# Performance work log

Hardware: AMD Instinct MI355X
Metric: run time of the kernel (lower is better)

Reference implementation:

```python
import jax, jax.numpy as jnp
import numpy as np

# Production-scale dims: CSA layer on a 64x64, 512-channel decoder feature map
B, C, H, W = 8, 512, 64, 64
HOLE = 32  # centered square hole side -> M = 1024 masked points, N = 3072 context points
EPS = 1e-8


def _mask_and_indices():
    m = np.zeros((H, W), np.float32)
    r0, c0 = (H - HOLE) // 2, (W - HOLE) // 2
    m[r0:r0 + HOLE, c0:c0 + HOLE] = 1.0
    flat = m.reshape(-1)
    mask_idx = np.nonzero(flat > 0.5)[0].astype(np.int32)      # masked (hole) flat positions, raster order
    nonmask_idx = np.nonzero(flat <= 0.5)[0].astype(np.int32)  # known (context) flat positions
    return m, nonmask_idx, mask_idx


def setup_inputs() -> dict:
    key = jax.random.key(0)
    x = jax.random.normal(key, (B, C, H, W), dtype=jnp.float32)
    m, nm, mi = _mask_and_indices()
    return {
        "input": x,
        "mask": jnp.asarray(m),
        "nonmask_point_idx": jnp.asarray(nm),
        "mask_point_idx": jnp.asarray(mi),
    }


def _csa(x, nonmask_point_idx, mask_point_idx):
    """Coherent Semantic Attention with 1x1 patches (shift_sz=1, stride=1).

    For each masked location (raster order): find the most-similar context
    patch by cosine similarity, then coherently blend it with the previously
    generated patch, weighted by their respective similarities.
    """
    b, c, h, w = x.shape
    feats = x.reshape(b, c, h * w)                      # [B,C,HW] 1x1 patches
    ctx = feats[:, :, nonmask_point_idx]                # [B,C,N] known/context patches
    msk = feats[:, :, mask_point_idx]                   # [B,C,M] masked patches
    ctx_n = ctx / (jnp.linalg.norm(ctx, axis=1, keepdims=True) + EPS)
    msk_n = msk / (jnp.linalg.norm(msk, axis=1, keepdims=True) + EPS)

    # cross cosine similarity: dominant compute (B*M*N*C)
    cos = jnp.einsum('bcm,bcn->bmn', msk_n, ctx_n)      # [B,M,N]
    maxc = cos.max(axis=-1)                             # [B,M] best context similarity
    amax = cos.argmax(axis=-1)                          # [B,M]
    # gather the best-matching (unnormalized) context patch per masked point
    best = jnp.take_along_axis(ctx.transpose(0, 2, 1), amax[..., None], axis=1)  # [B,M,C]

    xs = (msk_n.transpose(2, 0, 1),   # [M,B,C] normalized masked patches
          best.transpose(1, 0, 2),    # [M,B,C] best context patches
          maxc.T)                     # [M,B]

    def step(prev, inp):
        mn, bst, mx = inp
        prev_n = prev / (jnp.linalg.norm(prev, axis=-1, keepdims=True) + EPS)
        d_ad = jnp.maximum(jnp.sum(mn * prev_n, axis=-1), 0.0)   # [B] coherence with previous generated patch
        cur = (d_ad[:, None] * prev + mx[:, None] * bst) / (d_ad + mx + EPS)[:, None]
        return cur, cur

    # prev initialized to zeros -> d_ad = 0 for the first masked patch (pure context copy)
    _, gen = jax.lax.scan(step, jnp.zeros((b, c), x.dtype), xs)   # [M,B,C]

    out = feats.at[:, :, mask_point_idx].set(gen.transpose(1, 2, 0))
    return out.reshape(b, c, h, w)


def reference(input, mask, nonmask_point_idx, mask_point_idx):
    return _csa(input, nonmask_point_idx, mask_point_idx)
```

## Files before the change

### kernel.cpp

```cpp
#include <hip/hip_runtime.h>
#include <hip/hip_bf16.h>

#define B_   8
#define C_   512
#define HW_  4096
#define M_   1024
#define N_   3072
#define EPS_ 1e-8f

typedef __attribute__((ext_vector_type(4))) float f32x4;
typedef __attribute__((ext_vector_type(8))) short short8;

__global__ void k_norms(const float* __restrict__ x, float* __restrict__ inv_all) {
    int blk = blockIdx.x;
    int b = blk >> 5;
    int chunk = blk & 31;
    int hw = chunk * 128 + threadIdx.x;
    const float* xb = x + (size_t)b * C_ * HW_;
    float acc = 0.f;
#pragma unroll 8
    for (int c = 0; c < C_; ++c) {
        float v = xb[(size_t)c * HW_ + hw];
        acc = fmaf(v, v, acc);
    }
    inv_all[b * HW_ + hw] = 1.0f / (sqrtf(acc) + EPS_);
}

__global__ __launch_bounds__(256) void k_pack(const float* __restrict__ x,
    const int* __restrict__ nm_idx, const int* __restrict__ m_idx,
    const float* __restrict__ inv_all,
    unsigned int* __restrict__ Apk, unsigned int* __restrict__ Bpk,
    float* __restrict__ invM, float* __restrict__ invC)
{
    __shared__ float T[32][513];
    __shared__ int ps[32];
    int blk = blockIdx.x;
    int t = threadIdx.x;
    int isA = blk < 256;
    int b, grp;
    const int* idxarr;
    if (isA) { b = blk >> 5; grp = blk & 31; idxarr = m_idx; }
    else     { int r = blk - 256; b = r / 96; grp = r % 96; idxarr = nm_idx; }
    const float* xb = x + (size_t)b * C_ * HW_;
    if (t < 32) {
        int p = idxarr[grp * 32 + t];
        ps[t] = p;
        float iv = inv_all[b * HW_ + p];
        if (isA) invM[b * 1024 + grp * 32 + t] = iv;
        else     invC[b * 3072 + grp * 32 + t] = iv;
    }
    __syncthreads();
#pragma unroll 4
    for (int rep = 0; rep < 64; ++rep) {
        int idx = rep * 256 + t;
        int c = idx >> 5, i = idx & 31;
        T[i][c] = xb[(size_t)c * HW_ + ps[i]];
    }
    __syncthreads();
    unsigned int* dst = isA ? (Apk + ((size_t)b * 1024 + grp * 32) * 512)
                            : (Bpk + ((size_t)b * 3072 + grp * 32) * 512);
#pragma unroll 4
    for (int rep = 0; rep < 64; ++rep) {
        int idx = rep * 256 + t;
        int i = idx >> 9, c = idx & 511;
        float v = T[i][c];
        __hip_bfloat16 h = __float2bfloat16(v);
        float hf = __bfloat162float(h);
        __hip_bfloat16 l = __float2bfloat16(v - hf);
        unsigned int hi = __bfloat16_as_ushort(h);
        unsigned int lo = __bfloat16_as_ushort(l);
        dst[(size_t)i * 512 + c] = (lo << 16) | hi;
    }
}

__global__ __launch_bounds__(256, 2) void k_cosm(
    const unsigned int* __restrict__ Apk, const unsigned int* __restrict__ Bpk,
    const float* __restrict__ invM, const float* __restrict__ invC,
    float* __restrict__ pmax, int* __restrict__ pidx)
{
    __shared__ unsigned int As[128 * 36];
    __shared__ unsigned int Bs[128 * 36];
    __shared__ float sInvM[128];
    __shared__ float sInvC[128];

    int blk = blockIdx.x;
    int b  = blk / 192;
    int r  = blk % 192;
    int mt = r / 24;
    int nt = r % 24;
    int m0 = mt * 128, n0 = nt * 128;
    int t = threadIdx.x;
    int w = t >> 6, lane = t & 63;
    int wm = (w & 1) * 64, wn = (w >> 1) * 64;
    int quad = lane >> 4, nl = lane & 15;

    if (t < 128) sInvM[t] = invM[b * 1024 + m0 + t];
    else         sInvC[t - 128] = invC[b * 3072 + n0 + (t - 128)];

    const unsigned int* gA = Apk + ((size_t)b * 1024 + m0) * 512;
    const unsigned int* gB = Bpk + ((size_t)b * 3072 + n0) * 512;

    f32x4 acc[4][4];
#pragma unroll
    for (int i = 0; i < 4; ++i)
#pragma unroll
        for (int j = 0; j < 4; ++j) acc[i][j] = (f32x4){0.f, 0.f, 0.f, 0.f};

    for (int kt = 0; kt < 16; ++kt) {
        int k0 = kt * 32;
        __syncthreads();
#pragma unroll
        for (int rep = 0; rep < 4; ++rep) {
            int idx = rep * 1024 + t * 4;
            int row = idx >> 5, col = idx & 31;
            uint4 va = *(const uint4*)(gA + (size_t)row * 512 + k0 + col);
            uint4 vb = *(const uint4*)(gB + (size_t)row * 512 + k0 + col);
            *(uint4*)&As[row * 36 + col] = va;
            *(uint4*)&Bs[row * 36 + col] = vb;
        }
        __syncthreads();

        short8 ah[4], al[4], bh[4], bl[4];
#pragma unroll
        for (int mt2 = 0; mt2 < 4; ++mt2) {
            int m = wm + mt2 * 16 + nl;
            uint4 q0 = *(const uint4*)&As[m * 36 + quad * 8];
            uint4 q1 = *(const uint4*)&As[m * 36 + quad * 8 + 4];
            uint4 H, L;
            H.x = __builtin_amdgcn_perm(q0.y, q0.x, 0x05040100u);
            H.y = __builtin_amdgcn_perm(q0.w, q0.z, 0x05040100u);
            H.z = __builtin_amdgcn_perm(q1.y, q1.x, 0x05040100u);
            H.w = __builtin_amdgcn_perm(q1.w, q1.z, 0x05040100u);
            L.x = __builtin_amdgcn_perm(q0.y, q0.x, 0x07060302u);
            L.y = __builtin_amdgcn_perm(q0.w, q0.z, 0x07060302u);
            L.z = __builtin_amdgcn_perm(q1.y, q1.x, 0x07060302u);
            L.w = __builtin_amdgcn_perm(q1.w, q1.z, 0x07060302u);
            ah[mt2] = *(short8*)&H; al[mt2] = *(short8*)&L;
        }
#pragma unroll
        for (int nt2 = 0; nt2 < 4; ++nt2) {
            int n = wn + nt2 * 16 + nl;
            uint4 q0 = *(const uint4*)&Bs[n * 36 + quad * 8];
            uint4 q1 = *(const uint4*)&Bs[n * 36 + quad * 8 + 4];
            uint4 H, L;
            H.x = __builtin_amdgcn_perm(q0.y, q0.x, 0x05040100u);
            H.y = __builtin_amdgcn_perm(q0.w, q0.z, 0x05040100u);
            H.z = __builtin_amdgcn_perm(q1.y, q1.x, 0x05040100u);
            H.w = __builtin_amdgcn_perm(q1.w, q1.z, 0x05040100u);
            L.x = __builtin_amdgcn_perm(q0.y, q0.x, 0x07060302u);
            L.y = __builtin_amdgcn_perm(q0.w, q0.z, 0x07060302u);
            L.z = __builtin_amdgcn_perm(q1.y, q1.x, 0x07060302u);
            L.w = __builtin_amdgcn_perm(q1.w, q1.z, 0x07060302u);
            bh[nt2] = *(short8*)&H; bl[nt2] = *(short8*)&L;
        }
#pragma unroll
        for (int mt2 = 0; mt2 < 4; ++mt2)
#pragma unroll
            for (int nt2 = 0; nt2 < 4; ++nt2) {
                acc[mt2][nt2] = __builtin_amdgcn_mfma_f32_16x16x32_bf16(
                    ah[mt2], bh[nt2], acc[mt2][nt2], 0, 0, 0);
                acc[mt2][nt2] = __builtin_amdgcn_mfma_f32_16x16x32_bf16(
                    ah[mt2], bl[nt2], acc[mt2][nt2], 0, 0, 0);
                acc[mt2][nt2] = __builtin_amdgcn_mfma_f32_16x16x32_bf16(
                    al[mt2], bh[nt2], acc[mt2][nt2], 0, 0, 0);
            }
    }

#pragma unroll
    for (int mt2 = 0; mt2 < 4; ++mt2)
#pragma unroll
        for (int reg = 0; reg < 4; ++reg) {
            int ml = wm + mt2 * 16 + quad * 4 + reg;
            float im = sInvM[ml];
            float v1 = -3.402823466e38f, v2 = -3.402823466e38f;
            int i1 = 0x7fffffff, i2 = 0x7fffffff;
#pragma unroll
            for (int nt2 = 0; nt2 < 4; ++nt2) {
                int nlc = wn + nt2 * 16 + nl;
                float v = acc[mt2][nt2][reg] * im * sInvC[nlc];
                int n = n0 + nlc;
                if (v > v1 || (v == v1 && n < i1)) { v2 = v1; i2 = i1; v1 = v; i1 = n; }
                else if (v > v2 || (v == v2 && n < i2)) { v2 = v; i2 = n; }
            }
#pragma unroll
            for (int off = 1; off < 16; off <<= 1) {
                float o1v = __shfl_xor(v1, off, 64); int o1i = __shfl_xor(i1, off, 64);
                float o2v = __shfl_xor(v2, off, 64); int o2i = __shfl_xor(i2, off, 64);
                if (o1v > v1 || (o1v == v1 && o1i < i1)) { v2 = v1; i2 = i1; v1 = o1v; i1 = o1i; }
                else if (o1v > v2 || (o1v == v2 && o1i < i2)) { v2 = o1v; i2 = o1i; }
                if (o2v > v1 || (o2v == v1 && o2i < i1)) { v2 = v1; i2 = i1; v1 = o2v; i1 = o2i; }
                else if (o2v > v2 || (o2v == v2 && o2i < i2)) { v2 = o2v; i2 = o2i; }
            }
            if (nl == 0) {
                int m_glob = (b << 10) + m0 + ml;
                int slot = nt * 2 + (w >> 1);
                int o = (m_glob * 48 + slot) * 2;
                pmax[o + 0] = v1; pidx[o + 0] = i1;
                pmax[o + 1] = v2; pidx[o + 1] = i2;
            }
        }
}

__global__ void k_combine(const float* __restrict__ x,
    const int* __restrict__ nm_idx, const int* __restrict__ m_idx,
    const float* __restrict__ pmax, const int* __restrict__ pidx,
    float* __restrict__ maxc, int* __restrict__ bestp)
{
    int id = blockIdx.x * 256 + threadIdx.x;
    int b = id >> 10, m = id & 1023;
    float v1 = -3.402823466e38f, v2 = -3.402823466e38f;
    int i1 = 0x7fffffff, i2 = 0x7fffffff;
#pragma unroll 8
    for (int r = 0; r < 96; ++r) {
        float v = pmax[(size_t)id * 96 + r];
        int   n = pidx[(size_t)id * 96 + r];
        if (v > v1 || (v == v1 && n < i1)) { v2 = v1; i2 = i1; v1 = v; i1 = n; }
        else if (v > v2 || (v == v2 && n < i2)) { v2 = v; i2 = n; }
    }
    if (v1 - v2 < 1e-4f) {
        const float* xb = x + (size_t)b * C_ * HW_;
        int pm = m_idx[m], p1 = nm_idx[i1], p2 = nm_idx[i2];
        double smm = 0, s11 = 0, s22 = 0, sm1 = 0, sm2 = 0;
        for (int c = 0; c < C_; ++c) {
            double xm = xb[(size_t)c * HW_ + pm];
            double xa = xb[(size_t)c * HW_ + p1];
            double xc = xb[(size_t)c * HW_ + p2];
            smm += xm * xm; s11 += xa * xa; s22 += xc * xc;
            sm1 += xm * xa; sm2 += xm * xc;
        }
        double inv_m = 1.0 / (sqrt(smm) + 1e-8);
        double c1 = sm1 * inv_m / (sqrt(s11) + 1e-8);
        double c2 = sm2 * inv_m / (sqrt(s22) + 1e-8);
        if (c2 > c1 || (c2 == c1 && i2 < i1)) { v1 = v2; i1 = i2; }
    }
    maxc[id]  = v1;
    bestp[id] = nm_idx[i1];
}

__global__ void k_copy(const float4* __restrict__ in, float4* __restrict__ out) {
    int idx = blockIdx.x * 256 + threadIdx.x;
    int stride = gridDim.x * 256;
    for (int i = idx; i < (B_ * C_ * HW_ / 4); i += stride) out[i] = in[i];
}

__global__ __launch_bounds__(256) void k_gather(const float* __restrict__ x,
    const int* __restrict__ m_idx, const float* __restrict__ inv_all,
    const int* __restrict__ bestp, float* __restrict__ mskn, float* __restrict__ best)
{
    __shared__ float T[32][513];
    __shared__ int ps[32]; __shared__ float invm[32]; __shared__ int bp[32];
    int blk = blockIdx.x;
    int b = blk >> 5, row = blk & 31;
    int m0 = row * 32;
    int t = threadIdx.x;
    const float* xb = x + (size_t)b * C_ * HW_;
    if (t < 32) {
        int p = m_idx[m0 + t];
        ps[t] = p; invm[t] = inv_all[b * HW_ + p];
        bp[t] = bestp[(b << 10) + m0 + t];
    }
    __syncthreads();
#pragma unroll 4
    for (int rep = 0; rep < 64; ++rep) {
        int idx = rep * 256 + t;
        int c = idx >> 5, i = idx & 31;
        T[i][c] = xb[(size_t)c * HW_ + ps[i]];
    }
    __syncthreads();
#pragma unroll 4
    for (int rep = 0; rep < 64; ++rep) {
        int idx = rep * 256 + t;
        int i = idx >> 9, c = idx & 511;
        mskn[((size_t)(b << 10) + m0 + i) * C_ + c] = T[i][c] * invm[i];
    }
    for (int mi = 0; mi < 32; ++mi) {
        int p = bp[mi];
        size_t o = ((size_t)(b << 10) + m0 + mi) * C_;
        for (int c = t; c < C_; c += 256)
            best[o + c] = xb[(size_t)c * HW_ + p];
    }
}

__device__ __forceinline__ float wave_sum64(float x) {
    x += __int_as_float(__builtin_amdgcn_update_dpp(0, __float_as_int(x), 0x111, 0xf, 0xf, false));
    x += __int_as_float(__builtin_amdgcn_update_dpp(0, __float_as_int(x), 0x112, 0xf, 0xf, false));
    x += __int_as_float(__builtin_amdgcn_update_dpp(0, __float_as_int(x), 0x114, 0xf, 0xf, false));
    x += __int_as_float(__builtin_amdgcn_update_dpp(0, __float_as_int(x), 0x118, 0xf, 0xf, false));
    x += __int_as_float(__builtin_amdgcn_update_dpp(0, __float_as_int(x), 0x142, 0xa, 0xf, false));
    x += __int_as_float(__builtin_amdgcn_update_dpp(0, __float_as_int(x), 0x143, 0xc, 0xf, false));
    return __int_as_float(__builtin_amdgcn_readlane(__float_as_int(x), 63));
}

__device__ __forceinline__ void stage_slot(const float* gm, const float* gb,
                                           float* slot ) {
    typedef const __attribute__((address_space(1))) unsigned int GU;
    typedef __attribute__((address_space(3))) unsigned int LU;
    __builtin_amdgcn_global_load_lds((GU*)(gm),       (LU*)(slot),       16, 0, 0);
    __builtin_amdgcn_global_load_lds((GU*)(gm + 256), (LU*)(slot + 256), 16, 0, 0);
    __builtin_amdgcn_global_load_lds((GU*)(gb),       (LU*)(slot + 512), 16, 0, 0);
    __builtin_amdgcn_global_load_lds((GU*)(gb + 256), (LU*)(slot + 768), 16, 0, 0);
}

#define WAIT_VMCNT(N) asm volatile("s_waitcnt vmcnt(" #N ")" ::: "memory")

#define SCAN_STEP(mexpr, NLIT) do {                                          \
    int m_ = (mexpr);                                                        \
    if (m_ + 6 < M_)                                                         \
        stage_slot(mskn_b + (size_t)(m_ + 6) * 512 + lane * 4,               \
                   best_b + (size_t)(m_ + 6) * 512 + lane * 4,               \
                   &ring[((m_ + 6) & 7) << 10]);                             \
    WAIT_VMCNT(NLIT);                                                        \
    __builtin_amdgcn_sched_barrier(0);                                       \
    unsigned lb_ = ringBase + ((unsigned)(m_ & 7) << 12) + lane * 32u;       \
    f32x4 r0, r1, r2, r3;                                                    \
    asm volatile("ds_read_b128 %0, %4 offset:0\n\t"                          \
                 "ds_read_b128 %1, %4 offset:16\n\t"                         \
                 "ds_read_b128 %2, %4 offset:2048\n\t"                       \
                 "ds_read_b128 %3, %4 offset:2064\n\t"                       \
                 "s_waitcnt lgkmcnt(0)"                                      \
                 : "=&v"(r0), "=&v"(r1), "=&v"(r2), "=&v"(r3)                \
                 : "v"(lb_));                                                \
    __builtin_amdgcn_sched_barrier(0);                                       \
    float mn[8] = {r0.x, r0.y, r0.z, r0.w, r1.x, r1.y, r1.z, r1.w};          \
    float bs[8] = {r2.x, r2.y, r2.z, r2.w, r3.x, r3.y, r3.z, r3.w};          \
    float s1a = 0.f, s1b = 0.f, s2a = 0.f, s2b = 0.f;                        \
    _Pragma("unroll")                                                        \
    for (int j = 0; j < 4; ++j) {                                            \
        s1a = fmaf(pr[j], pr[j], s1a);                                       \
        s1b = fmaf(pr[j + 4], pr[j + 4], s1b);                               \
        s2a = fmaf(mn[j], pr[j], s2a);                                       \
        s2b = fmaf(mn[j + 4], pr[j + 4], s2b);                               \
    }                                                                        \
    float s1 = wave_sum64(s1a + s1b);                                        \
    float s2 = wave_sum64(s2a + s2b);                                        \
    float mxc = smx[m_];                                                     \
    float d_ad = fmaxf(s2, 0.f) * __builtin_amdgcn_rcpf(sqrtf(s1) + EPS_);   \
    float inv  = __builtin_amdgcn_rcpf(d_ad + mxc + EPS_);                   \
    _Pragma("unroll")                                                        \
    for (int j = 0; j < 8; ++j)                                              \
        pr[j] = (d_ad * pr[j] + mxc * bs[j]) * inv;                          \
    float4 o0 = {pr[0], pr[1], pr[2], pr[3]};                                \
    float4 o1 = {pr[4], pr[5], pr[6], pr[7]};                                \
    gen4[m_ * 128 + lane * 2]     = o0;                                      \
    gen4[m_ * 128 + lane * 2 + 1] = o1;                                      \
} while (0)

__global__ __launch_bounds__(64, 1) void k_scan(const float* __restrict__ mskn,
    const float* __restrict__ best, const float* __restrict__ maxc,
    float* __restrict__ gen)
{
    __shared__ float ring[8 * 1024];
    __shared__ float smx[M_];
    int b = blockIdx.x;
    int lane = threadIdx.x;
    const float* mskn_b = mskn + (size_t)b * M_ * C_;
    const float* best_b = best + (size_t)b * M_ * C_;
    const float* mx_p = maxc + b * M_;
    float4* gen4 = (float4*)(gen + (size_t)b * M_ * C_);

    unsigned ringBase = (unsigned)(size_t)(__attribute__((address_space(3))) float*)&ring[0];

#pragma unroll
    for (int i = 0; i < 16; ++i) smx[i * 64 + lane] = mx_p[i * 64 + lane];

    float pr[8];
#pragma unroll
    for (int j = 0; j < 8; ++j) pr[j] = 0.f;

#pragma unroll
    for (int s = 0; s < 6; ++s)
        stage_slot(mskn_b + (size_t)s * 512 + lane * 4,
                   best_b + (size_t)s * 512 + lane * 4,
                   &ring[(s & 7) << 10]);

    for (int mb = 0; mb < 127; ++mb) {
#pragma unroll
        for (int mi = 0; mi < 8; ++mi) {
            SCAN_STEP(mb * 8 + mi, 24);
        }
    }
#pragma unroll
    for (int mi = 0; mi < 8; ++mi) {
        SCAN_STEP(1016 + mi, 0);
    }
}

__global__ __launch_bounds__(256) void k_scatter(const float* __restrict__ gen,
    const int* __restrict__ m_idx, float* __restrict__ out)
{
    __shared__ float T[32][513];
    int blk = blockIdx.x;
    int b = blk >> 5, row = blk & 31;
    int m0 = row * 32;
    int t = threadIdx.x;
#pragma unroll 4
    for (int rep = 0; rep < 64; ++rep) {
        int idx = rep * 256 + t;
        int i = idx >> 9, c = idx & 511;
        T[i][c] = gen[((size_t)(b << 10) + m0 + i) * C_ + c];
    }
    __syncthreads();
    int colg = m_idx[m0];
    float* outb = out + (size_t)b * C_ * HW_;
#pragma unroll 4
    for (int rep = 0; rep < 64; ++rep) {
        int idx = rep * 256 + t;
        int c = idx >> 5, i = idx & 31;
        outb[(size_t)c * HW_ + colg + i] = T[i][c];
    }
}

extern "C" void kernel_launch(void* const* d_in, const int* in_sizes, int n_in,
                              void* d_out, int out_size, void* d_ws, size_t ws_size,
                              hipStream_t stream) {
    (void)in_sizes; (void)n_in; (void)out_size; (void)ws_size;
    const float* x      = (const float*)d_in[0];
    const int*   nm_idx = (const int*)d_in[2];
    const int*   m_idx  = (const int*)d_in[3];
    float* out = (float*)d_out;
    char* ws = (char*)d_ws;

    float* inv_all = (float*)(ws + 0);
    float* invM    = (float*)(ws + 131072);
    float* invC    = (float*)(ws + 163840);
    float* pmax    = (float*)(ws + 262144);
    int*   pidx    = (int*)  (ws + 3407872);
    float* maxc    = (float*)(ws + 6553600);
    int*   bestp   = (int*)  (ws + 6586368);
    unsigned int* Apk = (unsigned int*)(ws + 6619136);
    unsigned int* Bpk = (unsigned int*)(ws + 23396352);
    float* mskn = (float*)Apk;
    float* best = (float*)Bpk;
    float* gen  = (float*)(ws + 23396352 + 16777216);

    hipLaunchKernelGGL(k_norms,   dim3(256),  dim3(128), 0, stream, x, inv_all);
    hipLaunchKernelGGL(k_pack,    dim3(1024), dim3(256), 0, stream, x, nm_idx, m_idx, inv_all, Apk, Bpk, invM, invC);
    hipLaunchKernelGGL(k_cosm,    dim3(1536), dim3(256), 0, stream, Apk, Bpk, invM, invC, pmax, pidx);
    hipLaunchKernelGGL(k_combine, dim3(32),   dim3(256), 0, stream, x, nm_idx, m_idx, pmax, pidx, maxc, bestp);
    hipLaunchKernelGGL(k_copy,    dim3(2048), dim3(256), 0, stream, (const float4*)x, (float4*)out);
    hipLaunchKernelGGL(k_gather,  dim3(256),  dim3(256), 0, stream, x, m_idx, inv_all, bestp, mskn, best);
    hipLaunchKernelGGL(k_scan,    dim3(8),    dim3(64),  0, stream, mskn, best, maxc, gen);
    hipLaunchKernelGGL(k_scatter, dim3(256),  dim3(256), 0, stream, gen, m_idx, out);
}
```

Measured before the change: 736.2 us.

## Precompute Gram terms so scan reductions leave the serial critical path

Result: slower. 899.1 us (+22.1%).

```diff
diff --git a/kernel.cpp b/kernel.cpp
--- a/kernel.cpp
+++ b/kernel.cpp
@@ -291,6 +291,32 @@
     return __int_as_float(__builtin_amdgcn_readlane(__float_as_int(x), 63));
 }
 
+__global__ __launch_bounds__(64) void k_gram(const float* __restrict__ mskn,
+    const float* __restrict__ best, float* __restrict__ Bsq, float* __restrict__ Gmn)
+{
+    int id = blockIdx.x;
+    int b = id >> 10, m = id & 1023;
+    int lane = threadIdx.x;
+    const float4* bs4 = (const float4*)(best + ((size_t)b * M_ + m) * C_);
+    float4 b0 = bs4[lane * 2], b1 = bs4[lane * 2 + 1];
+    float sb = 0.f, sg = 0.f;
+    sb = fmaf(b0.x, b0.x, sb); sb = fmaf(b0.y, b0.y, sb);
+    sb = fmaf(b0.z, b0.z, sb); sb = fmaf(b0.w, b0.w, sb);
+    sb = fmaf(b1.x, b1.x, sb); sb = fmaf(b1.y, b1.y, sb);
+    sb = fmaf(b1.z, b1.z, sb); sb = fmaf(b1.w, b1.w, sb);
+    if (m + 1 < M_) {
+        const float4* mn4 = (const float4*)(mskn + ((size_t)b * M_ + m + 1) * C_);
+        float4 m0 = mn4[lane * 2], m1 = mn4[lane * 2 + 1];
+        sg = fmaf(m0.x, b0.x, sg); sg = fmaf(m0.y, b0.y, sg);
+        sg = fmaf(m0.z, b0.z, sg); sg = fmaf(m0.w, b0.w, sg);
+        sg = fmaf(m1.x, b1.x, sg); sg = fmaf(m1.y, b1.y, sg);
+        sg = fmaf(m1.z, b1.z, sg); sg = fmaf(m1.w, b1.w, sg);
+    }
+    sb = wave_sum64(sb);
+    sg = wave_sum64(sg);
+    if (lane == 0) { Bsq[id] = sb; Gmn[id] = sg; }
+}
+
 __device__ __forceinline__ void stage_slot(const float* gm, const float* gb,
                                            float* slot ) {
     typedef const __attribute__((address_space(1))) unsigned int GU;
@@ -305,83 +331,121 @@
 
 #define SCAN_STEP(mexpr, NLIT) do {                                          \
     int m_ = (mexpr);                                                        \
-    if (m_ + 6 < M_)                                                         \
-        stage_slot(mskn_b + (size_t)(m_ + 6) * 512 + lane * 4,               \
-                   best_b + (size_t)(m_ + 6) * 512 + lane * 4,               \
-                   &ring[((m_ + 6) & 7) << 10]);                             \
+    if (m_ + 7 < M_)                                                         \
+        stage_slot(mskn_b + (size_t)(m_ + 7) * 512 + lane * 4,               \
+                   best_b + (size_t)(m_ + 7) * 512 + lane * 4,               \
+                   &ring[((m_ + 7) & 7) << 10]);                             \
     WAIT_VMCNT(NLIT);                                                        \
     __builtin_amdgcn_sched_barrier(0);                                       \
-    unsigned lb_ = ringBase + ((unsigned)(m_ & 7) << 12) + lane * 32u;       \
-    f32x4 r0, r1, r2, r3;                                                    \
-    asm volatile("ds_read_b128 %0, %4 offset:0\n\t"                          \
-                 "ds_read_b128 %1, %4 offset:16\n\t"                         \
-                 "ds_read_b128 %2, %4 offset:2048\n\t"                       \
-                 "ds_read_b128 %3, %4 offset:2064\n\t"                       \
-                 "s_waitcnt lgkmcnt(0)"                                      \
-                 : "=&v"(r0), "=&v"(r1), "=&v"(r2), "=&v"(r3)                \
-                 : "v"(lb_));                                                \
-    __builtin_amdgcn_sched_barrier(0);                                       \
-    float mn[8] = {r0.x, r0.y, r0.z, r0.w, r1.x, r1.y, r1.z, r1.w};          \
-    float bs[8] = {r2.x, r2.y, r2.z, r2.w, r3.x, r3.y, r3.z, r3.w};          \
-    float s1a = 0.f, s1b = 0.f, s2a = 0.f, s2b = 0.f;                        \
+    int sl1 = ((m_ + 1 < M_) ? (m_ + 1) : (M_ - 1)) & 7;                     \
+    int sl2 = ((m_ + 2 < M_) ? (m_ + 2) : (M_ - 1)) & 7;                     \
+    float4 nb0 = *(float4*)&ring[sl1 * 1024 + 512 + lane * 8];               \
+    float4 nb1 = *(float4*)&ring[sl1 * 1024 + 512 + lane * 8 + 4];           \
+    float4 nm0 = *(float4*)&ring[sl2 * 1024 + lane * 8];                     \
+    float4 nm1 = *(float4*)&ring[sl2 * 1024 + lane * 8 + 4];                 \
+    float mxc = smx[m_];                                                     \
+    float Bm  = sB[m_];                                                      \
+    float Gm  = sG[m_];                                                      \
+    float d_ad = fmaxf(s2, 0.f) * __builtin_amdgcn_rcpf(sqrtf(s1) + EPS_);   \
+    float inv  = __builtin_amdgcn_rcpf(d_ad + mxc + EPS_);                   \
+    float al = d_ad * inv, be = mxc * inv;                                   \
+    _Pragma("unroll")                                                        \
+    for (int j = 0; j < 8; ++j)                                              \
+        pr[j] = fmaf(al, pr[j], be * bsn[j]);                                \
+                                    \
+    float s1n = fmaf(al * al, s1, fmaf(2.f * al * be, t1p, (be * be) * Bm)); \
+    float s2n = fmaf(al, t2p, be * Gm);                                      \
+    float4 o0 = {pr[0], pr[1], pr[2], pr[3]};                                \
+    float4 o1 = {pr[4], pr[5], pr[6], pr[7]};                                \
+    *(float4*)&genbuf[(m_ & 7) * 512 + lane * 8]     = o0;                   \
+    *(float4*)&genbuf[(m_ & 7) * 512 + lane * 8 + 4] = o1;                   \
+    float nb[8] = {nb0.x, nb0.y, nb0.z, nb0.w, nb1.x, nb1.y, nb1.z, nb1.w};  \
+    float nm[8] = {nm0.x, nm0.y, nm0.z, nm0.w, nm1.x, nm1.y, nm1.z, nm1.w};  \
+    float pa0 = 0.f, pa1 = 0.f, pb0 = 0.f, pb1 = 0.f;                        \
     _Pragma("unroll")                                                        \
     for (int j = 0; j < 4; ++j) {                                            \
-        s1a = fmaf(pr[j], pr[j], s1a);                                       \
-        s1b = fmaf(pr[j + 4], pr[j + 4], s1b);                               \
-        s2a = fmaf(mn[j], pr[j], s2a);                                       \
-        s2b = fmaf(mn[j + 4], pr[j + 4], s2b);                               \
+        pa0 = fmaf(pr[j], nb[j], pa0);                                       \
+        pa1 = fmaf(pr[j + 4], nb[j + 4], pa1);                               \
+        pb0 = fmaf(pr[j], nm[j], pb0);                                       \
+        pb1 = fmaf(pr[j + 4], nm[j + 4], pb1);                               \
     }                                                                        \
-    float s1 = wave_sum64(s1a + s1b);                                        \
-    float s2 = wave_sum64(s2a + s2b);                                        \
-    float mxc = smx[m_];                                                     \
-    float d_ad = fmaxf(s2, 0.f) * __builtin_amdgcn_rcpf(sqrtf(s1) + EPS_);   \
-    float inv  = __builtin_amdgcn_rcpf(d_ad + mxc + EPS_);                   \
+    t1p = wave_sum64(pa0 + pa1);                                             \
+    t2p = wave_sum64(pb0 + pb1);                                             \
+    s1 = s1n; s2 = s2n;                                                      \
     _Pragma("unroll")                                                        \
-    for (int j = 0; j < 8; ++j)                                              \
-        pr[j] = (d_ad * pr[j] + mxc * bs[j]) * inv;                          \
-    float4 o0 = {pr[0], pr[1], pr[2], pr[3]};                                \
-    float4 o1 = {pr[4], pr[5], pr[6], pr[7]};                                \
-    gen4[m_ * 128 + lane * 2]     = o0;                                      \
-    gen4[m_ * 128 + lane * 2 + 1] = o1;                                      \
+    for (int j = 0; j < 8; ++j) bsn[j] = nb[j];                              \
 } while (0)
 
 __global__ __launch_bounds__(64, 1) void k_scan(const float* __restrict__ mskn,
     const float* __restrict__ best, const float* __restrict__ maxc,
+    const float* __restrict__ Bsq, const float* __restrict__ Gmn,
     float* __restrict__ gen)
 {
     __shared__ float ring[8 * 1024];
     __shared__ float smx[M_];
+    __shared__ float sB[M_];
+    __shared__ float sG[M_];
+    __shared__ float genbuf[8 * 512];
     int b = blockIdx.x;
     int lane = threadIdx.x;
     const float* mskn_b = mskn + (size_t)b * M_ * C_;
     const float* best_b = best + (size_t)b * M_ * C_;
     const float* mx_p = maxc + b * M_;
+    const float* B_p  = Bsq + b * M_;
+    const float* G_p  = Gmn + b * M_;
     float4* gen4 = (float4*)(gen + (size_t)b * M_ * C_);
 
-    unsigned ringBase = (unsigned)(size_t)(__attribute__((address_space(3))) float*)&ring[0];
-
-#pragma unroll
-    for (int i = 0; i < 16; ++i) smx[i * 64 + lane] = mx_p[i * 64 + lane];
-
-    float pr[8];
-#pragma unroll
-    for (int j = 0; j < 8; ++j) pr[j] = 0.f;
-
-#pragma unroll
-    for (int s = 0; s < 6; ++s)
+#pragma unroll
+    for (int i = 0; i < 16; ++i) {
+        smx[i * 64 + lane] = mx_p[i * 64 + lane];
+        sB[i * 64 + lane]  = B_p[i * 64 + lane];
+        sG[i * 64 + lane]  = G_p[i * 64 + lane];
+    }
+    WAIT_VMCNT(0);
+    __builtin_amdgcn_sched_barrier(0);
+
+#pragma unroll
+    for (int s = 0; s < 7; ++s)
         stage_slot(mskn_b + (size_t)s * 512 + lane * 4,
                    best_b + (size_t)s * 512 + lane * 4,
                    &ring[(s & 7) << 10]);
+    WAIT_VMCNT(24);
+    __builtin_amdgcn_sched_barrier(0);
+
+    float pr[8], bsn[8];
+#pragma unroll
+    for (int j = 0; j < 8; ++j) pr[j] = 0.f;
+    {
+        float4 c0 = *(float4*)&ring[512 + lane * 8];
+        float4 c1 = *(float4*)&ring[512 + lane * 8 + 4];
+        bsn[0] = c0.x; bsn[1] = c0.y; bsn[2] = c0.z; bsn[3] = c0.w;
+        bsn[4] = c1.x; bsn[5] = c1.y; bsn[6] = c1.z; bsn[7] = c1.w;
+    }
+    float s1 = 0.f, s2 = 0.f, t1p = 0.f, t2p = 0.f;
 
     for (int mb = 0; mb < 127; ++mb) {
 #pragma unroll
         for (int mi = 0; mi < 8; ++mi) {
-            SCAN_STEP(mb * 8 + mi, 24);
+            SCAN_STEP(mb * 8 + mi, 20);
+        }
+#pragma unroll
+        for (int r = 0; r < 8; ++r) {
+            float4 fa = *(float4*)&genbuf[r * 512 + lane * 8];
+            float4 fb = *(float4*)&genbuf[r * 512 + lane * 8 + 4];
+            gen4[(mb * 8 + r) * 128 + lane * 2]     = fa;
+            gen4[(mb * 8 + r) * 128 + lane * 2 + 1] = fb;
         }
     }
 #pragma unroll
     for (int mi = 0; mi < 8; ++mi) {
         SCAN_STEP(1016 + mi, 0);
+    }
+#pragma unroll
+    for (int r = 0; r < 8; ++r) {
+        float4 fa = *(float4*)&genbuf[r * 512 + lane * 8];
+        float4 fb = *(float4*)&genbuf[r * 512 + lane * 8 + 4];
+        gen4[(1016 + r) * 128 + lane * 2]     = fa;
+        gen4[(1016 + r) * 128 + lane * 2 + 1] = fb;
     }
 }
 
@@ -432,6 +496,8 @@
     float* mskn = (float*)Apk;
     float* best = (float*)Bpk;
     float* gen  = (float*)(ws + 23396352 + 16777216);
+    float* Bsq  = (float*)(ws + 23396352 + 33554432);
+    float* Gmn  = (float*)(ws + 23396352 + 33554432 + 32768);
 
     hipLaunchKernelGGL(k_norms,   dim3(256),  dim3(128), 0, stream, x, inv_all);
     hipLaunchKernelGGL(k_pack,    dim3(1024), dim3(256), 0, stream, x, nm_idx, m_idx, inv_all, Apk, Bpk, invM, invC);
@@ -439,6 +505,7 @@
     hipLaunchKernelGGL(k_combine, dim3(32),   dim3(256), 0, stream, x, nm_idx, m_idx, pmax, pidx, maxc, bestp);
     hipLaunchKernelGGL(k_copy,    dim3(2048), dim3(256), 0, stream, (const float4*)x, (float4*)out);
     hipLaunchKernelGGL(k_gather,  dim3(256),  dim3(256), 0, stream, x, m_idx, inv_all, bestp, mskn, best);
-    hipLaunchKernelGGL(k_scan,    dim3(8),    dim3(64),  0, stream, mskn, best, maxc, gen);
+    hipLaunchKernelGGL(k_gram,    dim3(8192), dim3(64),  0, stream, mskn, best, Bsq, Gmn);
+    hipLaunchKernelGGL(k_scan,    dim3(8),    dim3(64),  0, stream, mskn, best, maxc, Bsq, Gmn, gen);
     hipLaunchKernelGGL(k_scatter, dim3(256),  dim3(256), 0, stream, gen, m_idx, out);
 }
```
